# Optimization experiments

Hardware: AMD Instinct MI355X
Metric: run time of the kernel (lower is better)

Reference implementation:

```python
import jax, jax.numpy as jnp
import numpy as np
import math

B, S = 4, 1024
N_ITEMS, EMB = 50000, 128
H, D = 4, 32


def setup_inputs() -> dict:
    key = jax.random.key(0)
    ks = jax.random.split(key, 12)

    def lin(k, fan_in, fan_out):
        lim = 1.0 / math.sqrt(fan_in)
        return jax.random.uniform(k, (fan_in, fan_out), minval=-lim, maxval=lim, dtype=jnp.float32)

    inp = {}
    inp["sequence_item_indices"] = jax.random.randint(ks[0], (B, S), 0, N_ITEMS, dtype=jnp.int32)
    inp["sequence_correct_flags"] = jax.random.randint(ks[1], (B, S), 0, 2, dtype=jnp.int32)
    inp["sequence_time_gaps"] = jax.random.uniform(ks[2], (B, S), dtype=jnp.float32) * 100.0
    inp["item_emb"] = jax.random.normal(ks[3], (N_ITEMS, EMB), dtype=jnp.float32) * 0.02
    inp["ans_emb"] = jax.random.normal(ks[4], (2, EMB), dtype=jnp.float32) * 0.02
    inp["Wq"] = lin(ks[5], EMB, H * D); inp["bq"] = jnp.zeros((H * D,), jnp.float32)
    inp["Wk"] = lin(ks[6], EMB, H * D); inp["bk"] = jnp.zeros((H * D,), jnp.float32)
    inp["Wv"] = lin(ks[7], EMB, H * D); inp["bv"] = jnp.zeros((H * D,), jnp.float32)
    inp["Wh"] = lin(ks[8], 2 * EMB, EMB); inp["bh"] = jnp.zeros((EMB,), jnp.float32)
    inp["W1"] = lin(ks[9], H * D + EMB, EMB); inp["b1"] = jnp.zeros((EMB,), jnp.float32)
    inp["W2"] = lin(ks[10], EMB, 1); inp["b2"] = jnp.zeros((1,), jnp.float32)
    inp["theta_raw"] = jnp.zeros((H,), jnp.float32)
    return inp


def reference(sequence_item_indices, sequence_correct_flags, sequence_time_gaps,
              item_emb, ans_emb, Wq, bq, Wk, bk, Wv, bv, Wh, bh, W1, b1, W2, b2, theta_raw):
    Bb, Ss = sequence_item_indices.shape
    Hn = theta_raw.shape[0]
    Dd = Wq.shape[1] // Hn

    e = item_emb[sequence_item_indices]                      # [B,S,E]
    a = ans_emb[sequence_correct_flags]                      # [B,S,E]
    inter = jnp.concatenate([e, a], axis=-1) @ Wh + bh       # history_projection

    Q = (e @ Wq + bq).reshape(Bb, Ss, Hn, Dd)
    K = (e @ Wk + bk).reshape(Bb, Ss, Hn, Dd)
    V = (inter @ Wv + bv).reshape(Bb, Ss, Hn, Dd)
    scale = 1.0 / jnp.sqrt(jnp.float32(Dd))

    # self relevance per history position; per-target softmax over i<t done via exclusive prefix sums
    sr = jnp.sum(Q * K, axis=-1) * scale                     # [B,S,H]
    ex = jnp.exp(sr - jnp.max(sr, axis=1, keepdims=True))    # shift-invariant
    Ep = jnp.concatenate([jnp.zeros((Bb, 1, Hn), sr.dtype), jnp.cumsum(ex, axis=1)], axis=1)  # [B,S+1,H]

    g = jnp.maximum(sequence_time_gaps.astype(jnp.float32), 1.0)
    Pp = jnp.concatenate([jnp.zeros((Bb, 1), g.dtype), jnp.cumsum(g, axis=1)], axis=1)        # [B,S+1]

    t = jnp.arange(1, Ss)                                    # targets, T = S-1
    i = jnp.arange(Ss)                                       # history positions
    mask = i[None, :] < t[:, None]                           # [T,S]
    step = (t[:, None] - i[None, :]).astype(jnp.float32)     # arange(L,0,-1)[i] == t - i
    gap_diff = Pp[:, 1:Ss, None] - Pp[:, None, :Ss]          # [B,T,S]  sum_{j in [i,t)} clamp(gap,1)
    Et = Ep[:, 1:Ss, :]                                      # [B,T,H]  softmax normalizer Z_t
    rel = (Et[:, :, None, :] - Ep[:, None, :Ss, :]) / Et[:, :, None, :]  # cumulative relevance [B,T,S,H]
    pd = jnp.where(mask[None, :, :, None],
                   step[None, :, :, None] * gap_diff[..., None] * rel, 0.0)  # perceived distance

    theta = jax.nn.softplus(theta_raw) + 1e-4                # [H]
    decay = jnp.exp(-theta * pd)                             # [B,T,S,H]

    # candidate query at position t equals query_projection(item_embedding[t])
    raw = jnp.einsum('bthd,bihd->btih', Q[:, 1:], K) * scale # [B,T,S,H]
    scores = jnp.where(mask[None, :, :, None], raw * decay, -1e30)
    attn = jax.nn.softmax(scores, axis=2)                    # softmax over history positions
    ctx = jnp.einsum('btih,bihd->bthd', attn, V).reshape(Bb, Ss - 1, Hn * Dd)

    feat = jnp.concatenate([ctx, e[:, 1:]], axis=-1)
    h1 = jax.nn.relu(feat @ W1 + b1)                         # dropout is inference identity
    logit = (h1 @ W2 + b2)[..., 0]
    pred = jax.nn.sigmoid(logit)                             # [B,S-1]
    valid = jnp.ones((Bb, Ss - 1), dtype=bool)               # all positions valid (no padding)
    return pred, valid
```

## Files before the change

kernel.cpp:

```cpp
#include <hip/hip_runtime.h>
#include <math.h>

#define BSZ 4
#define SSZ 1024
#define EMBD 128
#define HN 4
#define DN 32
#define TQ (SSZ - 1)
#define NROWS (BSZ * TQ)

typedef __attribute__((ext_vector_type(8))) short bf16x8;
typedef __attribute__((ext_vector_type(4))) short bf16x4;
typedef __attribute__((ext_vector_type(4))) float f32x4;

static __device__ __forceinline__ unsigned short f2bf(float x) {
    union { float f; unsigned u; } v; v.f = x;
    unsigned r = v.u + 0x7fffu + ((v.u >> 16) & 1u);
    return (unsigned short)(r >> 16);
}
static __device__ __forceinline__ bf16x8 cvt8(const float4 a, const float4 b) {
    bf16x8 v;
    v[0] = (short)f2bf(a.x); v[1] = (short)f2bf(a.y);
    v[2] = (short)f2bf(a.z); v[3] = (short)f2bf(a.w);
    v[4] = (short)f2bf(b.x); v[5] = (short)f2bf(b.y);
    v[6] = (short)f2bf(b.z); v[7] = (short)f2bf(b.w);
    return v;
}

__global__ __launch_bounds__(256)
void embed3_kernel(const int* __restrict__ idx, const int* __restrict__ flg,
                   const float* __restrict__ item_emb, const float* __restrict__ ans_emb,
                   const float* __restrict__ Wq, const float* __restrict__ bq,
                   const float* __restrict__ Wk, const float* __restrict__ bk,
                   const float* __restrict__ Wv, const float* __restrict__ bv,
                   const float* __restrict__ Wh, const float* __restrict__ bh_bias,
                   float* __restrict__ Qt, float* __restrict__ Kt, float* __restrict__ Vt,
                   float* __restrict__ ec, float* __restrict__ srw)
{
    __shared__ __align__(16) unsigned short esb[16][136];
    __shared__ __align__(16) unsigned short asb[16][136];
    __shared__ __align__(16) unsigned short intb[16][136];
    __shared__ __align__(16) unsigned short Wt[128][40];

    const int tid = threadIdx.x;
    const int tok0 = blockIdx.x * 16;
    const int b = blockIdx.x >> 6;
    const int s0 = tok0 & 1023;
    const int w = tid >> 6, lane = tid & 63;
    const int quad = lane >> 4, col = lane & 15;

    {
        const int tk = tid >> 4;
        const int d0 = (tid & 15) * 8;
        const int tok = tok0 + tk;
        const float* esrc = item_emb + (size_t)idx[tok] * EMBD + d0;
        const float* asrc = ans_emb + (size_t)flg[tok] * EMBD + d0;
        const float4 e0 = *(const float4*)esrc;
        const float4 e1 = *(const float4*)(esrc + 4);
        const float4 a0 = *(const float4*)asrc;
        const float4 a1 = *(const float4*)(asrc + 4);
        *(float4*)(ec + (size_t)tok * EMBD + d0) = e0;
        *(float4*)(ec + (size_t)tok * EMBD + d0 + 4) = e1;
        *(bf16x8*)&esb[tk][d0] = cvt8(e0, e1);
        *(bf16x8*)&asb[tk][d0] = cvt8(a0, a1);
    }

    const int jb = (tid & 31) * 4;
    const int ib = (tid >> 5) * 4;
    #define STAGE_W(SRC)                                                     \
    {                                                                        \
        float rr[4][4];                                                      \
        *(float4*)rr[0] = *(const float4*)((SRC) + (ib + 0) * 128 + jb);     \
        *(float4*)rr[1] = *(const float4*)((SRC) + (ib + 1) * 128 + jb);     \
        *(float4*)rr[2] = *(const float4*)((SRC) + (ib + 2) * 128 + jb);     \
        *(float4*)rr[3] = *(const float4*)((SRC) + (ib + 3) * 128 + jb);     \
        _Pragma("unroll")                                                    \
        for (int jj = 0; jj < 4; jj++) {                                     \
            bf16x4 v;                                                        \
            v[0] = (short)f2bf(rr[0][jj]); v[1] = (short)f2bf(rr[1][jj]);    \
            v[2] = (short)f2bf(rr[2][jj]); v[3] = (short)f2bf(rr[3][jj]);    \
            *(bf16x4*)&Wt[jb + jj][ib] = v;                                  \
        }                                                                    \
    }

    f32x4 accI[2] = {{0.f,0.f,0.f,0.f},{0.f,0.f,0.f,0.f}};
    for (int kc = 0; kc < 8; kc++) {
        __syncthreads();
        STAGE_W(Wh + (size_t)kc * 32 * 128);
        __syncthreads();
        const unsigned short (*Asrc)[136] = (kc < 4) ? esb : asb;
        const bf16x8 af = *(const bf16x8*)&Asrc[col][(kc & 3) * 32 + quad * 8];
        #pragma unroll
        for (int ntl = 0; ntl < 2; ntl++) {
            const bf16x8 bf = *(const bf16x8*)&Wt[w * 32 + ntl * 16 + col][quad * 8];
            accI[ntl] = __builtin_amdgcn_mfma_f32_16x16x32_bf16(af, bf, accI[ntl], 0, 0, 0);
        }
    }
    #pragma unroll
    for (int ntl = 0; ntl < 2; ntl++) {
        const int j = w * 32 + ntl * 16 + col;
        const float bb = bh_bias[j];
        #pragma unroll
        for (int r = 0; r < 4; r++)
            intb[quad * 4 + r][j] = f2bf(accI[ntl][r] + bb);
    }

    f32x4 accQ[2] = {{0.f,0.f,0.f,0.f},{0.f,0.f,0.f,0.f}};
    f32x4 accK[2] = {{0.f,0.f,0.f,0.f},{0.f,0.f,0.f,0.f}};
    for (int kc = 0; kc < 4; kc++) {
        __syncthreads();
        STAGE_W(Wq + (size_t)kc * 32 * 128);
        __syncthreads();
        const bf16x8 af = *(const bf16x8*)&esb[col][kc * 32 + quad * 8];
        #pragma unroll
        for (int ntl = 0; ntl < 2; ntl++) {
            const bf16x8 bf = *(const bf16x8*)&Wt[w * 32 + ntl * 16 + col][quad * 8];
            accQ[ntl] = __builtin_amdgcn_mfma_f32_16x16x32_bf16(af, bf, accQ[ntl], 0, 0, 0);
        }
    }
    for (int kc = 0; kc < 4; kc++) {
        __syncthreads();
        STAGE_W(Wk + (size_t)kc * 32 * 128);
        __syncthreads();
        const bf16x8 af = *(const bf16x8*)&esb[col][kc * 32 + quad * 8];
        #pragma unroll
        for (int ntl = 0; ntl < 2; ntl++) {
            const bf16x8 bf = *(const bf16x8*)&Wt[w * 32 + ntl * 16 + col][quad * 8];
            accK[ntl] = __builtin_amdgcn_mfma_f32_16x16x32_bf16(af, bf, accK[ntl], 0, 0, 0);
        }
    }

    const int bhn = b * HN + w;
    {
        float p[4] = {0.f, 0.f, 0.f, 0.f};
        #pragma unroll
        for (int ntl = 0; ntl < 2; ntl++) {
            const int j = w * 32 + ntl * 16 + col;
            const float bQ = bq[j], bK = bk[j];
            #pragma unroll
            for (int r = 0; r < 4; r++) {
                const float qv = accQ[ntl][r] + bQ;
                const float kv = accK[ntl][r] + bK;
                const int s = s0 + quad * 4 + r;
                Qt[((size_t)bhn * SSZ + s) * DN + ntl * 16 + col] = qv;
                Kt[((size_t)bhn * SSZ + s) * DN + ntl * 16 + col] = kv;
                p[r] = fmaf(qv, kv, p[r]);
            }
        }
        #pragma unroll
        for (int r = 0; r < 4; r++) {
            float pr = p[r];
            pr += __shfl_xor(pr, 1, 64);
            pr += __shfl_xor(pr, 2, 64);
            pr += __shfl_xor(pr, 4, 64);
            pr += __shfl_xor(pr, 8, 64);
            if (col == 0)
                srw[(size_t)bhn * SSZ + s0 + quad * 4 + r] = pr * 0.17677669529663687f;
        }
    }

    f32x4 accV[2] = {{0.f,0.f,0.f,0.f},{0.f,0.f,0.f,0.f}};
    for (int kc = 0; kc < 4; kc++) {
        __syncthreads();
        STAGE_W(Wv + (size_t)kc * 32 * 128);
        __syncthreads();
        const bf16x8 af = *(const bf16x8*)&intb[col][kc * 32 + quad * 8];
        #pragma unroll
        for (int ntl = 0; ntl < 2; ntl++) {
            const bf16x8 bf = *(const bf16x8*)&Wt[w * 32 + ntl * 16 + col][quad * 8];
            accV[ntl] = __builtin_amdgcn_mfma_f32_16x16x32_bf16(af, bf, accV[ntl], 0, 0, 0);
        }
    }
    #pragma unroll
    for (int ntl = 0; ntl < 2; ntl++) {
        const int j = w * 32 + ntl * 16 + col;
        const float bV = bv[j];
        #pragma unroll
        for (int r = 0; r < 4; r++) {
            const int s = s0 + quad * 4 + r;
            Vt[((size_t)bhn * SSZ + s) * DN + ntl * 16 + col] = accV[ntl][r] + bV;
        }
    }
    #undef STAGE_W
}

__global__ __launch_bounds__(1024)
void scan_kernel(const float* __restrict__ srw, const float* __restrict__ gaps,
                 float* __restrict__ Ep, float* __restrict__ Pp)
{
    __shared__ float buf[SSZ];
    __shared__ float red[16];
    const int tid = threadIdx.x;

    if (blockIdx.x < 16) {
        const int bh = blockIdx.x;
        float v = srw[bh * SSZ + tid];
        float wm = v;
        #pragma unroll
        for (int msk = 32; msk >= 1; msk >>= 1) wm = fmaxf(wm, __shfl_xor(wm, msk, 64));
        if ((tid & 63) == 0) red[tid >> 6] = wm;
        __syncthreads();
        if (tid == 0) {
            float mm = red[0];
            for (int k = 1; k < 16; k++) mm = fmaxf(mm, red[k]);
            red[0] = mm;
        }
        __syncthreads();
        const float mx = red[0];

        buf[tid] = __expf(v - mx);
        __syncthreads();
        for (int off = 1; off < SSZ; off <<= 1) {
            float tv = (tid >= off) ? buf[tid - off] : 0.0f;
            __syncthreads();
            buf[tid] += tv;
            __syncthreads();
        }
        Ep[bh * (SSZ + 1) + tid + 1] = buf[tid];
        if (tid == 0) Ep[bh * (SSZ + 1)] = 0.0f;
    } else {
        const int b = blockIdx.x - 16;
        buf[tid] = fmaxf(gaps[b * SSZ + tid], 1.0f);
        __syncthreads();
        for (int off = 1; off < SSZ; off <<= 1) {
            float tv = (tid >= off) ? buf[tid - off] : 0.0f;
            __syncthreads();
            buf[tid] += tv;
            __syncthreads();
        }
        Pp[b * (SSZ + 1) + tid + 1] = buf[tid];
        if (tid == 0) Pp[b * (SSZ + 1)] = 0.0f;
    }
}

__global__ __launch_bounds__(256)
void attn_mfma_kernel(const float* __restrict__ Qt, const float* __restrict__ Kt,
                      const float* __restrict__ Vt,
                      const float* __restrict__ Ep, const float* __restrict__ Pp,
                      const float* __restrict__ theta_raw, float* __restrict__ csw)
{
    __shared__ __align__(16) unsigned short Qs[64][40];
    __shared__ __align__(16) unsigned short Ks[64][40];
    __shared__ __align__(16) unsigned short Vs[32][72];
    __shared__ __align__(16) unsigned short Ps[4][16][72];
    __shared__ float EpS[SSZ + 1];
    __shared__ float PpS[SSZ + 1];

    const int bid = blockIdx.x;
    const int qt = bid & 15;
    const int bh = bid >> 4;
    const int b = bh >> 2, h = bh & 3;
    const int tid = threadIdx.x;
    const int w = tid >> 6, lane = tid & 63;
    const int quad = lane >> 4, col = lane & 15;
    const int t0 = qt * 64 + 1;
    const float scale = 0.17677669529663687f;

    {
        const float* Epb = Ep + bh * (SSZ + 1);
        const float* Ppb = Pp + b * (SSZ + 1);
        for (int x = tid; x <= SSZ; x += 256) { EpS[x] = Epb[x]; PpS[x] = Ppb[x]; }
    }
    {
        const int qq = tid >> 2;
        const int d0 = (tid & 3) * 8;
        int t = t0 + qq; if (t > 1023) t = 1023;
        const float* src = Qt + ((size_t)(bh * SSZ + t)) * DN + d0;
        bf16x8 v;
        #pragma unroll
        for (int k = 0; k < 8; k++) v[k] = (short)f2bf(src[k] * scale);
        *(bf16x8*)&Qs[qq][d0] = v;
    }
    __syncthreads();

    const float theta = logf(1.0f + __expf(theta_raw[h])) + 1e-4f;
    const float nth = -theta;
    float Ept[4], Ppt[4], iEp[4], tft[4];
    int qrow[4], tq[4];
    #pragma unroll
    for (int r = 0; r < 4; r++) {
        qrow[r] = w * 16 + quad * 4 + r;
        tq[r] = t0 + qrow[r];
        tft[r] = (float)tq[r];
        Ept[r] = EpS[tq[r]];
        Ppt[r] = PpS[tq[r]];
        iEp[r] = 1.0f / Ept[r];
    }

    const bf16x8 aq = *(const bf16x8*)&Qs[w * 16 + col][quad * 8];

    f32x4 acc0 = {0.f, 0.f, 0.f, 0.f};
    f32x4 acc1 = {0.f, 0.f, 0.f, 0.f};
    float lsum[4] = {0.f, 0.f, 0.f, 0.f};

    for (int c = 0; c <= qt; c++) {
        __syncthreads();
        {
            const int i = tid >> 2;
            const int d0 = (tid & 3) * 8;
            const float* src = Kt + ((size_t)(bh * SSZ + c * 64 + i)) * DN + d0;
            bf16x8 v;
            #pragma unroll
            for (int k = 0; k < 8; k++) v[k] = (short)f2bf(src[k]);
            *(bf16x8*)&Ks[i][d0] = v;
        }
        {
            const int i = tid >> 2;
            const int d0 = (tid & 3) * 8;
            const float* src = Vt + ((size_t)(bh * SSZ + c * 64 + i)) * DN + d0;
            #pragma unroll
            for (int k = 0; k < 8; k++) Vs[d0 + k][i] = f2bf(src[k]);
        }
        __syncthreads();

        const bool full = (c < qt);
        #pragma unroll
        for (int nt = 0; nt < 4; nt++) {
            const bf16x8 bk = *(const bf16x8*)&Ks[nt * 16 + col][quad * 8];
            f32x4 z = {0.f, 0.f, 0.f, 0.f};
            f32x4 raw = __builtin_amdgcn_mfma_f32_16x16x32_bf16(aq, bk, z, 0, 0, 0);
            const int il = nt * 16 + col;
            const int i_ = c * 64 + il;
            const float Epi = EpS[i_];
            const float Ppi = PpS[i_];
            const float fi = (float)i_;
            #pragma unroll
            for (int r = 0; r < 4; r++) {
                const float pdv = (tft[r] - fi) * (Ppt[r] - Ppi) * ((Ept[r] - Epi) * iEp[r]);
                const float sc  = raw[r] * __expf(nth * pdv);
                float p = __expf(sc);
                p = (full || il <= qrow[r]) ? p : 0.0f;
                lsum[r] += p;
                Ps[w][quad * 4 + r][il] = f2bf(p);
            }
        }
        #pragma unroll
        for (int ks = 0; ks < 2; ks++) {
            const bf16x8 ap = *(const bf16x8*)&Ps[w][col][ks * 32 + quad * 8];
            const bf16x8 bv0 = *(const bf16x8*)&Vs[col][ks * 32 + quad * 8];
            const bf16x8 bv1 = *(const bf16x8*)&Vs[16 + col][ks * 32 + quad * 8];
            acc0 = __builtin_amdgcn_mfma_f32_16x16x32_bf16(ap, bv0, acc0, 0, 0, 0);
            acc1 = __builtin_amdgcn_mfma_f32_16x16x32_bf16(ap, bv1, acc1, 0, 0, 0);
        }
    }

    #pragma unroll
    for (int r = 0; r < 4; r++) {
        float lr = lsum[r];
        #pragma unroll
        for (int msk = 8; msk >= 1; msk >>= 1) lr += __shfl_xor(lr, msk, 64);
        lsum[r] = 1.0f / lr;
    }

    #pragma unroll
    for (int r = 0; r < 4; r++) {
        if (tq[r] <= 1023) {
            float* dst = csw + ((size_t)(b * TQ + (tq[r] - 1))) * EMBD + h * DN;
            dst[col]      = acc0[r] * lsum[r];
            dst[16 + col] = acc1[r] * lsum[r];
        }
    }
}

__global__ __launch_bounds__(256)
void mlp3_kernel(const float* __restrict__ csw, const float* __restrict__ ec,
                 const float* __restrict__ W1, const float* __restrict__ b1,
                 const float* __restrict__ W2, const float* __restrict__ b2,
                 float* __restrict__ out)
{
    __shared__ __align__(16) unsigned short featb[32][264];
    __shared__ __align__(16) unsigned short W1t[128][264];
    __shared__ float sred[4][16];

    const int tid = threadIdx.x;
    const int r0 = blockIdx.x * 32;
    const int w = tid >> 6, lane = tid & 63;
    const int quad = lane >> 4, col = lane & 15;
    const int mt = w & 1, nh = w >> 1;

    {
        const int jb = (tid & 31) * 4;
        const int ib = (tid >> 5) * 4;
        for (int ic = 0; ic < 8; ic++) {
            const int i0 = ic * 32 + ib;
            float rr[4][4];
            *(float4*)rr[0] = *(const float4*)(W1 + (size_t)(i0 + 0) * 128 + jb);
            *(float4*)rr[1] = *(const float4*)(W1 + (size_t)(i0 + 1) * 128 + jb);
            *(float4*)rr[2] = *(const float4*)(W1 + (size_t)(i0 + 2) * 128 + jb);
            *(float4*)rr[3] = *(const float4*)(W1 + (size_t)(i0 + 3) * 128 + jb);
            #pragma unroll
            for (int jj = 0; jj < 4; jj++) {
                bf16x4 v;
                v[0] = (short)f2bf(rr[0][jj]); v[1] = (short)f2bf(rr[1][jj]);
                v[2] = (short)f2bf(rr[2][jj]); v[3] = (short)f2bf(rr[3][jj]);
                *(bf16x4*)&W1t[jb + jj][i0] = v;
            }
        }
    }
    {
        const int rr = tid >> 3;
        const int c0 = (tid & 7) * 32;
        int row = r0 + rr; if (row >= NROWS) row = NROWS - 1;
        const float* src;
        if (c0 < 128) {
            src = csw + (size_t)row * EMBD + c0;
        } else {
            const int bb = row / TQ;
            const int tt = row - bb * TQ + 1;
            src = ec + ((size_t)(bb * SSZ + tt)) * EMBD + (c0 - 128);
        }
        #pragma unroll
        for (int g = 0; g < 4; g++) {
            const float4 f0 = ((const float4*)src)[g * 2];
            const float4 f1 = ((const float4*)src)[g * 2 + 1];
            *(bf16x8*)&featb[rr][c0 + g * 8] = cvt8(f0, f1);
        }
    }
    __syncthreads();

    float s[4] = {0.f, 0.f, 0.f, 0.f};
    #pragma unroll
    for (int ntl = 0; ntl < 4; ntl++) {
        const int nt = nh * 4 + ntl;
        f32x4 acc = {0.f, 0.f, 0.f, 0.f};
        #pragma unroll
        for (int kc = 0; kc < 8; kc++) {
            const bf16x8 af = *(const bf16x8*)&featb[mt * 16 + col][kc * 32 + quad * 8];
            const bf16x8 bf = *(const bf16x8*)&W1t[nt * 16 + col][kc * 32 + quad * 8];
            acc = __builtin_amdgcn_mfma_f32_16x16x32_bf16(af, bf, acc, 0, 0, 0);
        }
        const int j = nt * 16 + col;
        const float b1j = b1[j], w2j = W2[j];
        #pragma unroll
        for (int r = 0; r < 4; r++)
            s[r] = fmaf(fmaxf(acc[r] + b1j, 0.0f), w2j, s[r]);
    }
    #pragma unroll
    for (int r = 0; r < 4; r++) {
        float sr = s[r];
        sr += __shfl_xor(sr, 1, 64);
        sr += __shfl_xor(sr, 2, 64);
        sr += __shfl_xor(sr, 4, 64);
        sr += __shfl_xor(sr, 8, 64);
        if (col == 0) sred[w][quad * 4 + r] = sr;
    }
    __syncthreads();
    if (tid < 32) {
        const int mt2 = tid >> 4, rr = tid & 15;
        const float logit = sred[mt2][rr] + sred[mt2 + 2][rr] + b2[0];
        const int grow = r0 + tid;
        if (grow < NROWS) {
            out[grow] = 1.0f / (1.0f + __expf(-logit));
            out[NROWS + grow] = 1.0f;
        }
    }
}

extern "C" void kernel_launch(void* const* d_in, const int* in_sizes, int n_in,
                              void* d_out, int out_size, void* d_ws, size_t ws_size,
                              hipStream_t stream)
{
    const int*   idx       = (const int*)d_in[0];
    const int*   flg       = (const int*)d_in[1];
    const float* gaps      = (const float*)d_in[2];
    const float* item_emb  = (const float*)d_in[3];
    const float* ans_emb   = (const float*)d_in[4];
    const float* Wq        = (const float*)d_in[5];
    const float* bq        = (const float*)d_in[6];
    const float* Wk        = (const float*)d_in[7];
    const float* bk        = (const float*)d_in[8];
    const float* Wv        = (const float*)d_in[9];
    const float* bv        = (const float*)d_in[10];
    const float* Wh        = (const float*)d_in[11];
    const float* bh        = (const float*)d_in[12];
    const float* W1        = (const float*)d_in[13];
    const float* b1        = (const float*)d_in[14];
    const float* W2        = (const float*)d_in[15];
    const float* b2        = (const float*)d_in[16];
    const float* theta_raw = (const float*)d_in[17];

    float* ws  = (float*)d_ws;
    float* Qt  = ws;
    float* Kt  = Qt + BSZ * HN * SSZ * DN;
    float* Vt  = Kt + BSZ * HN * SSZ * DN;
    float* ec  = Vt + BSZ * HN * SSZ * DN;
    float* srw = ec + BSZ * SSZ * EMBD;
    float* Ep  = srw + BSZ * HN * SSZ;
    float* Pp  = Ep + 16416;
    float* csw = Pp + 4128;
    (void)ws_size;

    float* out = (float*)d_out;

    embed3_kernel<<<BSZ * SSZ / 16, 256, 0, stream>>>(
        idx, flg, item_emb, ans_emb, Wq, bq, Wk, bk, Wv, bv, Wh, bh,
        Qt, Kt, Vt, ec, srw);
    scan_kernel<<<20, 1024, 0, stream>>>(srw, gaps, Ep, Pp);
    attn_mfma_kernel<<<BSZ * HN * 16, 256, 0, stream>>>(
        Qt, Kt, Vt, Ep, Pp, theta_raw, csw);
    mlp3_kernel<<<(NROWS + 31) / 32, 256, 0, stream>>>(
        csw, ec, W1, b1, W2, b2, out);
}
```

Baseline: 158.5 us.

## Fold prefix scans into attention kernel and store Q/K/V as bf16

Removes the separate scan kernel. Each attention block now computes the exp prefix sums and the gap prefix sums itself, using wave shuffle scans into shared memory. The embedding kernel writes Q (pre-scaled), K and V directly as bf16 rather than fp32, so the attention kernel no longer converts them per tile. The weight staging in the embedding kernel is merged into one 20-round loop that prefetches the next weight slice into registers. The attention loop also prefetches the next K/V tile into registers. The scan is repeated in every query-tile block, and the exp no longer subtracts the max, so large scores could overflow.

```diff
diff --git a/kernel.cpp b/kernel.cpp
--- a/kernel.cpp
+++ b/kernel.cpp
@@ -28,13 +28,14 @@
 }
 
 __global__ __launch_bounds__(256)
-void embed3_kernel(const int* __restrict__ idx, const int* __restrict__ flg,
+void embed4_kernel(const int* __restrict__ idx, const int* __restrict__ flg,
                    const float* __restrict__ item_emb, const float* __restrict__ ans_emb,
                    const float* __restrict__ Wq, const float* __restrict__ bq,
                    const float* __restrict__ Wk, const float* __restrict__ bk,
                    const float* __restrict__ Wv, const float* __restrict__ bv,
                    const float* __restrict__ Wh, const float* __restrict__ bh_bias,
-                   float* __restrict__ Qt, float* __restrict__ Kt, float* __restrict__ Vt,
+                   unsigned short* __restrict__ Qts, unsigned short* __restrict__ Kts,
+                   unsigned short* __restrict__ Vts,
                    float* __restrict__ ec, float* __restrict__ srw)
 {
     __shared__ __align__(16) unsigned short esb[16][136];
@@ -67,184 +68,114 @@
 
     const int jb = (tid & 31) * 4;
     const int ib = (tid >> 5) * 4;
-    #define STAGE_W(SRC)                                                     \
-    {                                                                        \
-        float rr[4][4];                                                      \
-        *(float4*)rr[0] = *(const float4*)((SRC) + (ib + 0) * 128 + jb);     \
-        *(float4*)rr[1] = *(const float4*)((SRC) + (ib + 1) * 128 + jb);     \
-        *(float4*)rr[2] = *(const float4*)((SRC) + (ib + 2) * 128 + jb);     \
-        *(float4*)rr[3] = *(const float4*)((SRC) + (ib + 3) * 128 + jb);     \
-        _Pragma("unroll")                                                    \
-        for (int jj = 0; jj < 4; jj++) {                                     \
-            bf16x4 v;                                                        \
-            v[0] = (short)f2bf(rr[0][jj]); v[1] = (short)f2bf(rr[1][jj]);    \
-            v[2] = (short)f2bf(rr[2][jj]); v[3] = (short)f2bf(rr[3][jj]);    \
-            *(bf16x4*)&Wt[jb + jj][ib] = v;                                  \
-        }                                                                    \
+    float rr[4][4];
+
+    #define WSRC(R) ((R) < 8 ? Wh + (size_t)(R) * 4096                     \
+                  : (R) < 12 ? Wq + (size_t)((R) - 8) * 4096               \
+                  : (R) < 16 ? Wk + (size_t)((R) - 12) * 4096              \
+                  : Wv + (size_t)((R) - 16) * 4096)
+    #define LOADW(P)                                                       \
+    {                                                                      \
+        const float* _p = (P);                                             \
+        *(float4*)rr[0] = *(const float4*)(_p + (ib + 0) * 128 + jb);      \
+        *(float4*)rr[1] = *(const float4*)(_p + (ib + 1) * 128 + jb);      \
+        *(float4*)rr[2] = *(const float4*)(_p + (ib + 2) * 128 + jb);      \
+        *(float4*)rr[3] = *(const float4*)(_p + (ib + 3) * 128 + jb);      \
+    }
+    #define STOREW                                                         \
+    {                                                                      \
+        _Pragma("unroll")                                                  \
+        for (int jj = 0; jj < 4; jj++) {                                   \
+            bf16x4 v;                                                      \
+            v[0] = (short)f2bf(rr[0][jj]); v[1] = (short)f2bf(rr[1][jj]);  \
+            v[2] = (short)f2bf(rr[2][jj]); v[3] = (short)f2bf(rr[3][jj]);  \
+            *(bf16x4*)&Wt[jb + jj][ib] = v;                                \
+        }                                                                  \
     }
 
     f32x4 accI[2] = {{0.f,0.f,0.f,0.f},{0.f,0.f,0.f,0.f}};
-    for (int kc = 0; kc < 8; kc++) {
-        __syncthreads();
-        STAGE_W(Wh + (size_t)kc * 32 * 128);
-        __syncthreads();
-        const unsigned short (*Asrc)[136] = (kc < 4) ? esb : asb;
-        const bf16x8 af = *(const bf16x8*)&Asrc[col][(kc & 3) * 32 + quad * 8];
+    f32x4 accQ[2] = {{0.f,0.f,0.f,0.f},{0.f,0.f,0.f,0.f}};
+    f32x4 accK[2] = {{0.f,0.f,0.f,0.f},{0.f,0.f,0.f,0.f}};
+    f32x4 accV[2] = {{0.f,0.f,0.f,0.f},{0.f,0.f,0.f,0.f}};
+
+    LOADW(WSRC(0));
+    #pragma unroll
+    for (int r = 0; r < 20; r++) {
+        __syncthreads();
+        STOREW;
+        __syncthreads();
+        if (r < 19) LOADW(WSRC(r + 1));
+
+        const unsigned short (*Ab)[136] = (r < 4) ? esb : (r < 8) ? asb
+                                        : (r < 16) ? esb : intb;
+        const int koff = ((r < 8) ? (r & 3) : (r < 12) ? (r - 8)
+                        : (r < 16) ? (r - 12) : (r - 16)) * 32;
+        const bf16x8 af = *(const bf16x8*)&Ab[col][koff + quad * 8];
+        f32x4* acc = (r < 8) ? accI : (r < 12) ? accQ : (r < 16) ? accK : accV;
         #pragma unroll
         for (int ntl = 0; ntl < 2; ntl++) {
             const bf16x8 bf = *(const bf16x8*)&Wt[w * 32 + ntl * 16 + col][quad * 8];
-            accI[ntl] = __builtin_amdgcn_mfma_f32_16x16x32_bf16(af, bf, accI[ntl], 0, 0, 0);
-        }
-    }
+            acc[ntl] = __builtin_amdgcn_mfma_f32_16x16x32_bf16(af, bf, acc[ntl], 0, 0, 0);
+        }
+        if (r == 7) {
+            #pragma unroll
+            for (int ntl = 0; ntl < 2; ntl++) {
+                const int j = w * 32 + ntl * 16 + col;
+                const float bb = bh_bias[j];
+                #pragma unroll
+                for (int r4 = 0; r4 < 4; r4++)
+                    intb[quad * 4 + r4][j] = f2bf(accI[ntl][r4] + bb);
+            }
+        }
+    }
+    #undef LOADW
+    #undef STOREW
+    #undef WSRC
+
+    const int bhn = b * HN + w;
+    const float scale = 0.17677669529663687f;
+    float p[4] = {0.f, 0.f, 0.f, 0.f};
     #pragma unroll
     for (int ntl = 0; ntl < 2; ntl++) {
         const int j = w * 32 + ntl * 16 + col;
-        const float bb = bh_bias[j];
-        #pragma unroll
-        for (int r = 0; r < 4; r++)
-            intb[quad * 4 + r][j] = f2bf(accI[ntl][r] + bb);
-    }
-
-    f32x4 accQ[2] = {{0.f,0.f,0.f,0.f},{0.f,0.f,0.f,0.f}};
-    f32x4 accK[2] = {{0.f,0.f,0.f,0.f},{0.f,0.f,0.f,0.f}};
-    for (int kc = 0; kc < 4; kc++) {
-        __syncthreads();
-        STAGE_W(Wq + (size_t)kc * 32 * 128);
-        __syncthreads();
-        const bf16x8 af = *(const bf16x8*)&esb[col][kc * 32 + quad * 8];
-        #pragma unroll
-        for (int ntl = 0; ntl < 2; ntl++) {
-            const bf16x8 bf = *(const bf16x8*)&Wt[w * 32 + ntl * 16 + col][quad * 8];
-            accQ[ntl] = __builtin_amdgcn_mfma_f32_16x16x32_bf16(af, bf, accQ[ntl], 0, 0, 0);
-        }
-    }
-    for (int kc = 0; kc < 4; kc++) {
-        __syncthreads();
-        STAGE_W(Wk + (size_t)kc * 32 * 128);
-        __syncthreads();
-        const bf16x8 af = *(const bf16x8*)&esb[col][kc * 32 + quad * 8];
-        #pragma unroll
-        for (int ntl = 0; ntl < 2; ntl++) {
-            const bf16x8 bf = *(const bf16x8*)&Wt[w * 32 + ntl * 16 + col][quad * 8];
-            accK[ntl] = __builtin_amdgcn_mfma_f32_16x16x32_bf16(af, bf, accK[ntl], 0, 0, 0);
-        }
-    }
-
-    const int bhn = b * HN + w;
-    {
-        float p[4] = {0.f, 0.f, 0.f, 0.f};
-        #pragma unroll
-        for (int ntl = 0; ntl < 2; ntl++) {
-            const int j = w * 32 + ntl * 16 + col;
-            const float bQ = bq[j], bK = bk[j];
-            #pragma unroll
-            for (int r = 0; r < 4; r++) {
-                const float qv = accQ[ntl][r] + bQ;
-                const float kv = accK[ntl][r] + bK;
-                const int s = s0 + quad * 4 + r;
-                Qt[((size_t)bhn * SSZ + s) * DN + ntl * 16 + col] = qv;
-                Kt[((size_t)bhn * SSZ + s) * DN + ntl * 16 + col] = kv;
-                p[r] = fmaf(qv, kv, p[r]);
-            }
-        }
+        const float bQ = bq[j], bK = bk[j], bV = bv[j];
         #pragma unroll
         for (int r = 0; r < 4; r++) {
-            float pr = p[r];
-            pr += __shfl_xor(pr, 1, 64);
-            pr += __shfl_xor(pr, 2, 64);
-            pr += __shfl_xor(pr, 4, 64);
-            pr += __shfl_xor(pr, 8, 64);
-            if (col == 0)
-                srw[(size_t)bhn * SSZ + s0 + quad * 4 + r] = pr * 0.17677669529663687f;
-        }
-    }
-
-    f32x4 accV[2] = {{0.f,0.f,0.f,0.f},{0.f,0.f,0.f,0.f}};
-    for (int kc = 0; kc < 4; kc++) {
-        __syncthreads();
-        STAGE_W(Wv + (size_t)kc * 32 * 128);
-        __syncthreads();
-        const bf16x8 af = *(const bf16x8*)&intb[col][kc * 32 + quad * 8];
-        #pragma unroll
-        for (int ntl = 0; ntl < 2; ntl++) {
-            const bf16x8 bf = *(const bf16x8*)&Wt[w * 32 + ntl * 16 + col][quad * 8];
-            accV[ntl] = __builtin_amdgcn_mfma_f32_16x16x32_bf16(af, bf, accV[ntl], 0, 0, 0);
-        }
-    }
-    #pragma unroll
-    for (int ntl = 0; ntl < 2; ntl++) {
-        const int j = w * 32 + ntl * 16 + col;
-        const float bV = bv[j];
-        #pragma unroll
-        for (int r = 0; r < 4; r++) {
+            const float qv = accQ[ntl][r] + bQ;
+            const float kv = accK[ntl][r] + bK;
             const int s = s0 + quad * 4 + r;
-            Vt[((size_t)bhn * SSZ + s) * DN + ntl * 16 + col] = accV[ntl][r] + bV;
-        }
-    }
-    #undef STAGE_W
-}
-
-__global__ __launch_bounds__(1024)
-void scan_kernel(const float* __restrict__ srw, const float* __restrict__ gaps,
-                 float* __restrict__ Ep, float* __restrict__ Pp)
+            const size_t o = ((size_t)bhn * SSZ + s) * DN + ntl * 16 + col;
+            Qts[o] = f2bf(qv * scale);
+            Kts[o] = f2bf(kv);
+            Vts[o] = f2bf(accV[ntl][r] + bV);
+            p[r] = fmaf(qv, kv, p[r]);
+        }
+    }
+    #pragma unroll
+    for (int r = 0; r < 4; r++) {
+        float pr = p[r];
+        pr += __shfl_xor(pr, 1, 64);
+        pr += __shfl_xor(pr, 2, 64);
+        pr += __shfl_xor(pr, 4, 64);
+        pr += __shfl_xor(pr, 8, 64);
+        if (col == 0)
+            srw[(size_t)bhn * SSZ + s0 + quad * 4 + r] = pr * scale;
+    }
+}
+
+__global__ __launch_bounds__(256)
+void attn4_kernel(const unsigned short* __restrict__ Qts,
+                  const unsigned short* __restrict__ Kts,
+                  const unsigned short* __restrict__ Vts,
+                  const float* __restrict__ srw, const float* __restrict__ gaps,
+                  const float* __restrict__ theta_raw, float* __restrict__ csw)
 {
-    __shared__ float buf[SSZ];
-    __shared__ float red[16];
-    const int tid = threadIdx.x;
-
-    if (blockIdx.x < 16) {
-        const int bh = blockIdx.x;
-        float v = srw[bh * SSZ + tid];
-        float wm = v;
-        #pragma unroll
-        for (int msk = 32; msk >= 1; msk >>= 1) wm = fmaxf(wm, __shfl_xor(wm, msk, 64));
-        if ((tid & 63) == 0) red[tid >> 6] = wm;
-        __syncthreads();
-        if (tid == 0) {
-            float mm = red[0];
-            for (int k = 1; k < 16; k++) mm = fmaxf(mm, red[k]);
-            red[0] = mm;
-        }
-        __syncthreads();
-        const float mx = red[0];
-
-        buf[tid] = __expf(v - mx);
-        __syncthreads();
-        for (int off = 1; off < SSZ; off <<= 1) {
-            float tv = (tid >= off) ? buf[tid - off] : 0.0f;
-            __syncthreads();
-            buf[tid] += tv;
-            __syncthreads();
-        }
-        Ep[bh * (SSZ + 1) + tid + 1] = buf[tid];
-        if (tid == 0) Ep[bh * (SSZ + 1)] = 0.0f;
-    } else {
-        const int b = blockIdx.x - 16;
-        buf[tid] = fmaxf(gaps[b * SSZ + tid], 1.0f);
-        __syncthreads();
-        for (int off = 1; off < SSZ; off <<= 1) {
-            float tv = (tid >= off) ? buf[tid - off] : 0.0f;
-            __syncthreads();
-            buf[tid] += tv;
-            __syncthreads();
-        }
-        Pp[b * (SSZ + 1) + tid + 1] = buf[tid];
-        if (tid == 0) Pp[b * (SSZ + 1)] = 0.0f;
-    }
-}
-
-__global__ __launch_bounds__(256)
-void attn_mfma_kernel(const float* __restrict__ Qt, const float* __restrict__ Kt,
-                      const float* __restrict__ Vt,
-                      const float* __restrict__ Ep, const float* __restrict__ Pp,
-                      const float* __restrict__ theta_raw, float* __restrict__ csw)
-{
-    __shared__ __align__(16) unsigned short Qs[64][40];
     __shared__ __align__(16) unsigned short Ks[64][40];
     __shared__ __align__(16) unsigned short Vs[32][72];
     __shared__ __align__(16) unsigned short Ps[4][16][72];
     __shared__ float EpS[SSZ + 1];
     __shared__ float PpS[SSZ + 1];
+    __shared__ float wtot[4];
 
     const int bid = blockIdx.x;
     const int qt = bid & 15;
@@ -254,22 +185,52 @@
     const int w = tid >> 6, lane = tid & 63;
     const int quad = lane >> 4, col = lane & 15;
     const int t0 = qt * 64 + 1;
-    const float scale = 0.17677669529663687f;
-
-    {
-        const float* Epb = Ep + bh * (SSZ + 1);
-        const float* Ppb = Pp + b * (SSZ + 1);
-        for (int x = tid; x <= SSZ; x += 256) { EpS[x] = Epb[x]; PpS[x] = Ppb[x]; }
-    }
-    {
-        const int qq = tid >> 2;
-        const int d0 = (tid & 3) * 8;
-        int t = t0 + qq; if (t > 1023) t = 1023;
-        const float* src = Qt + ((size_t)(bh * SSZ + t)) * DN + d0;
-        bf16x8 v;
-        #pragma unroll
-        for (int k = 0; k < 8; k++) v[k] = (short)f2bf(src[k] * scale);
-        *(bf16x8*)&Qs[qq][d0] = v;
+
+    {
+        const float4 sv = *(const float4*)(srw + (size_t)bh * SSZ + tid * 4);
+        const float e0 = __expf(sv.x);
+        const float p0 = e0;
+        const float p1 = p0 + __expf(sv.y);
+        const float p2 = p1 + __expf(sv.z);
+        const float p3 = p2 + __expf(sv.w);
+        float s = p3;
+        #pragma unroll
+        for (int d = 1; d < 64; d <<= 1) {
+            const float t = __shfl_up(s, d, 64);
+            if (lane >= d) s += t;
+        }
+        if (lane == 63) wtot[w] = s;
+        __syncthreads();
+        float base = s - p3;
+        for (int ww = 0; ww < w; ww++) base += wtot[ww];
+        EpS[tid * 4 + 1] = base + p0;
+        EpS[tid * 4 + 2] = base + p1;
+        EpS[tid * 4 + 3] = base + p2;
+        EpS[tid * 4 + 4] = base + p3;
+        if (tid == 0) EpS[0] = 0.0f;
+    }
+    {
+        const float4 gv = *(const float4*)(gaps + (size_t)b * SSZ + tid * 4);
+        const float p0 = fmaxf(gv.x, 1.0f);
+        const float p1 = p0 + fmaxf(gv.y, 1.0f);
+        const float p2 = p1 + fmaxf(gv.z, 1.0f);
+        const float p3 = p2 + fmaxf(gv.w, 1.0f);
+        float s = p3;
+        #pragma unroll
+        for (int d = 1; d < 64; d <<= 1) {
+            const float t = __shfl_up(s, d, 64);
+            if (lane >= d) s += t;
+        }
+        __syncthreads();
+        if (lane == 63) wtot[w] = s;
+        __syncthreads();
+        float base = s - p3;
+        for (int ww = 0; ww < w; ww++) base += wtot[ww];
+        PpS[tid * 4 + 1] = base + p0;
+        PpS[tid * 4 + 2] = base + p1;
+        PpS[tid * 4 + 3] = base + p2;
+        PpS[tid * 4 + 4] = base + p3;
+        if (tid == 0) PpS[0] = 0.0f;
     }
     __syncthreads();
 
@@ -287,31 +248,32 @@
         iEp[r] = 1.0f / Ept[r];
     }
 
-    const bf16x8 aq = *(const bf16x8*)&Qs[w * 16 + col][quad * 8];
+    bf16x8 aq;
+    {
+        int t = t0 + w * 16 + col; if (t > 1023) t = 1023;
+        aq = *(const bf16x8*)(Qts + ((size_t)(bh * SSZ + t)) * DN + quad * 8);
+    }
 
     f32x4 acc0 = {0.f, 0.f, 0.f, 0.f};
     f32x4 acc1 = {0.f, 0.f, 0.f, 0.f};
     float lsum[4] = {0.f, 0.f, 0.f, 0.f};
 
+    const int i_st = tid >> 2;
+    const int d0 = (tid & 3) * 8;
+    bf16x8 kreg = *(const bf16x8*)(Kts + ((size_t)(bh * SSZ + i_st)) * DN + d0);
+    bf16x8 vreg = *(const bf16x8*)(Vts + ((size_t)(bh * SSZ + i_st)) * DN + d0);
+
     for (int c = 0; c <= qt; c++) {
         __syncthreads();
-        {
-            const int i = tid >> 2;
-            const int d0 = (tid & 3) * 8;
-            const float* src = Kt + ((size_t)(bh * SSZ + c * 64 + i)) * DN + d0;
-            bf16x8 v;
-            #pragma unroll
-            for (int k = 0; k < 8; k++) v[k] = (short)f2bf(src[k]);
-            *(bf16x8*)&Ks[i][d0] = v;
-        }
-        {
-            const int i = tid >> 2;
-            const int d0 = (tid & 3) * 8;
-            const float* src = Vt + ((size_t)(bh * SSZ + c * 64 + i)) * DN + d0;
-            #pragma unroll
-            for (int k = 0; k < 8; k++) Vs[d0 + k][i] = f2bf(src[k]);
-        }
-        __syncthreads();
+        *(bf16x8*)&Ks[i_st][d0] = kreg;
+        #pragma unroll
+        for (int k2 = 0; k2 < 8; k2++) Vs[d0 + k2][i_st] = (unsigned short)vreg[k2];
+        __syncthreads();
+        if (c < qt) {
+            const size_t o = ((size_t)(bh * SSZ + (c + 1) * 64 + i_st)) * DN + d0;
+            kreg = *(const bf16x8*)(Kts + o);
+            vreg = *(const bf16x8*)(Vts + o);
+        }
 
         const bool full = (c < qt);
         #pragma unroll
@@ -351,7 +313,6 @@
         for (int msk = 8; msk >= 1; msk >>= 1) lr += __shfl_xor(lr, msk, 64);
         lsum[r] = 1.0f / lr;
     }
-
     #pragma unroll
     for (int r = 0; r < 4; r++) {
         if (tq[r] <= 1023) {
@@ -478,26 +439,23 @@
     const float* W2        = (const float*)d_in[15];
     const float* b2        = (const float*)d_in[16];
     const float* theta_raw = (const float*)d_in[17];
-
-    float* ws  = (float*)d_ws;
-    float* Qt  = ws;
-    float* Kt  = Qt + BSZ * HN * SSZ * DN;
-    float* Vt  = Kt + BSZ * HN * SSZ * DN;
-    float* ec  = Vt + BSZ * HN * SSZ * DN;
-    float* srw = ec + BSZ * SSZ * EMBD;
-    float* Ep  = srw + BSZ * HN * SSZ;
-    float* Pp  = Ep + 16416;
-    float* csw = Pp + 4128;
-    (void)ws_size;
+    (void)in_sizes; (void)n_in; (void)ws_size;
+
+    const size_t QKV = (size_t)BSZ * HN * SSZ * DN;
+    unsigned short* Qts = (unsigned short*)d_ws;
+    unsigned short* Kts = Qts + QKV;
+    unsigned short* Vts = Kts + QKV;
+    float* ec  = (float*)(Vts + QKV);
+    float* srw = ec + (size_t)BSZ * SSZ * EMBD;
+    float* csw = srw + (size_t)BSZ * HN * SSZ;
 
     float* out = (float*)d_out;
 
-    embed3_kernel<<<BSZ * SSZ / 16, 256, 0, stream>>>(
+    embed4_kernel<<<BSZ * SSZ / 16, 256, 0, stream>>>(
         idx, flg, item_emb, ans_emb, Wq, bq, Wk, bk, Wv, bv, Wh, bh,
-        Qt, Kt, Vt, ec, srw);
-    scan_kernel<<<20, 1024, 0, stream>>>(srw, gaps, Ep, Pp);
-    attn_mfma_kernel<<<BSZ * HN * 16, 256, 0, stream>>>(
-        Qt, Kt, Vt, Ep, Pp, theta_raw, csw);
+        Qts, Kts, Vts, ec, srw);
+    attn4_kernel<<<BSZ * HN * 16, 256, 0, stream>>>(
+        Qts, Kts, Vts, srw, gaps, theta_raw, csw);
     mlp3_kernel<<<(NROWS + 31) / 32, 256, 0, stream>>>(
         csw, ec, W1, b1, W2, b2, out);
 }
```

Result: faster. 149.4 us (-5.7%).
